# Kernel optimization log

Hardware: AMD Instinct MI355X
Metric: run time of the kernel (lower is better)

The kernel has to match this reference:

```python
import jax, jax.numpy as jnp
import numpy as np

B, L, E, H = 2, 2048, 1024, 16
HD = E // H          # head_dim = 64
G = H // 4           # heads per kernel-size group = 4


def _dwconv(x, w, b):
    """Causal depthwise conv. x: (B, G, L, D); w: (D, k); b: (D,).
    Matches PadLeft(k-1) + Conv1d(D, D, k, groups=D): y[l] = sum_j w[:, j] * x[l - (k-1) + j] + b."""
    k = w.shape[-1]
    Lx = x.shape[2]
    xp = jnp.pad(x, ((0, 0), (0, 0), (k - 1, 0), (0, 0)))
    out = b
    for j in range(k):
        out = out + xp[:, :, j:j + Lx, :] * w[:, j]
    return out


def setup_inputs() -> dict:
    key = jax.random.key(0)
    ks = jax.random.split(key, 32)
    s = 0.02
    inp = {"x": jax.random.normal(ks[0], (B, L, E), jnp.float32)}
    for i, n in enumerate(["Wq", "Wk", "Wv", "Wo"]):
        inp[n] = jax.random.normal(ks[1 + i], (E, E), jnp.float32) * s
    inp["bo"] = jax.random.normal(ks[5], (E,), jnp.float32) * s
    i = 6
    for ksz in (3, 5, 7):
        for pfx in ("q", "k", "v"):
            inp[f"{pfx}{ksz}_w"] = jax.random.normal(ks[i], (HD, ksz), jnp.float32) * (1.0 / ksz)
            inp[f"{pfx}{ksz}_b"] = jax.random.normal(ks[i + 1], (HD,), jnp.float32) * s
            i += 2
    return inp


def reference(x, Wq, Wk, Wv, Wo, bo,
              q3_w, q3_b, k3_w, k3_b, v3_w, v3_b,
              q5_w, q5_b, k5_w, k5_b, v5_w, v5_b,
              q7_w, q7_b, k7_w, k7_b, v7_w, v7_b):
    b, l, _ = x.shape

    def split(t):  # (b, l, E) -> (b, 4, G, l, HD)
        return t.reshape(b, l, 4, G, HD).transpose(0, 2, 3, 1, 4)

    q = split(x @ Wq.T)
    k = split(x @ Wk.T)
    v = split(x @ Wv.T)

    # NOTE: faithful to source quirks -- k and v convs are applied to the
    # (already convolved) q group, not to k/v.
    q0, k0, v0 = q[:, 0], k[:, 0], v[:, 0]
    q1 = _dwconv(q[:, 1], q3_w, q3_b)
    k1 = _dwconv(q1, k3_w, k3_b)
    v1 = _dwconv(q1, v3_w, v3_b)
    q2 = _dwconv(q[:, 2], q5_w, q5_b)
    k2 = _dwconv(q2, k5_w, k5_b)
    v2 = _dwconv(q2, v5_w, v5_b)
    q3 = _dwconv(q[:, 3], q7_w, q7_b)
    k3 = _dwconv(q3, k7_w, k7_b)
    v3 = _dwconv(q3, v7_w, v7_b)

    Q = jnp.concatenate([q0, q1, q2, q3], axis=1)  # (b, H, l, HD)
    K = jnp.concatenate([k0, k1, k2, k3], axis=1)
    V = jnp.concatenate([v0, v1, v2, v3], axis=1)

    logit = jnp.einsum('bnid,bnjd->bnij', Q, K) * (HD ** -0.5)
    attn = jax.nn.softmax(logit, axis=-1)
    attn_out = jnp.einsum('bnij,bnjd->bnid', attn, V)

    # Source quirk: output uses rearranged V, discarding attn_out.
    out = V.transpose(0, 2, 1, 3).reshape(b, l, E)
    # keep the attention compute alive without changing the math
    out = out + 0.0 * attn_out.transpose(0, 2, 1, 3).reshape(b, l, E)
    return out @ Wo.T + bo
```

## Files before the change

kernel.cpp:

```cpp
#include <hip/hip_runtime.h>
#include <hip/hip_bf16.h>
#include <stdint.h>

#define L_SEQ 2048
#define MTOT  4096
#define EDIM  1024

typedef __attribute__((ext_vector_type(8))) short bf16x8;
typedef __attribute__((ext_vector_type(4))) float f32x4;
typedef __attribute__((ext_vector_type(4))) float float4v;
typedef __attribute__((ext_vector_type(4))) unsigned short us4;
typedef __attribute__((ext_vector_type(2))) unsigned int u32x2;

__device__ __forceinline__ unsigned short f2b(float f) {
    union { float f; unsigned u; } v; v.f = f;
    return (unsigned short)((v.u + 0x7FFFu + ((v.u >> 16) & 1u)) >> 16);
}
__device__ __forceinline__ float b2f(unsigned short h) {
    union { unsigned u; float f; } v; v.u = ((unsigned)h) << 16;
    return v.f;
}

__device__ __forceinline__ void lds16(const void* g, void* l) {
    __builtin_amdgcn_global_load_lds((const __attribute__((address_space(1))) void*)g,
                                     (__attribute__((address_space(3))) void*)l, 16, 0, 0);
}

__global__ __launch_bounds__(256) void prep_kernel(
    const float* __restrict__ x, const float* __restrict__ Wq,
    const float* __restrict__ Wv, const float* __restrict__ Wo,
    unsigned short* __restrict__ xb, unsigned short* __restrict__ W1b,
    unsigned short* __restrict__ Wob,
    const float* __restrict__ q3w, const float* __restrict__ q3b,
    const float* __restrict__ v3w, const float* __restrict__ v3b,
    const float* __restrict__ q5w, const float* __restrict__ q5b,
    const float* __restrict__ v5w, const float* __restrict__ v5b,
    const float* __restrict__ q7w, const float* __restrict__ q7b,
    const float* __restrict__ v7w, const float* __restrict__ v7b,
    float* __restrict__ H, float* __restrict__ Beff, float* __restrict__ Corr)
{
    const int XQ = (MTOT * EDIM) / 4;
    const int WQ = (EDIM * EDIM) / 4;
    if (blockIdx.x >= 6144) {
        int ch = (blockIdx.x - 6144) * 256 + threadIdx.x;
        int g = ch >> 8;
        int d = ch & 63;
        int k = 3 + 2 * g;
        const float* qw = (g == 0) ? q3w : (g == 1) ? q5w : q7w;
        const float* qb = (g == 0) ? q3b : (g == 1) ? q5b : q7b;
        const float* vw = (g == 0) ? v3w : (g == 1) ? v5w : v7w;
        const float* vb = (g == 0) ? v3b : (g == 1) ? v5b : v7b;

        float hq[7], hv[7];
        for (int i = 0; i < 7; ++i) { hq[i] = 0.f; hv[i] = 0.f; }
        for (int i = 0; i < k; ++i) {
            hq[i] = qw[d * k + (k - 1 - i)];
            hv[i] = vw[d * k + (k - 1 - i)];
        }
        float h[13];
        for (int i = 0; i < 13; ++i) h[i] = 0.f;
        for (int a = 0; a < 7; ++a)
            for (int b = 0; b < 7; ++b)
                h[a + b] += hq[a] * hv[b];
        for (int i = 0; i < 13; ++i) H[i * 768 + ch] = h[i];

        float sv = 0.f;
        for (int j = 0; j < k; ++j) sv += vw[d * k + j];
        Beff[ch] = qb[d] * sv + vb[d];

        for (int l = 0; l < 6; ++l) {
            float s2 = 0.f;
            for (int i = l + 1; i < 7; ++i) s2 += hv[i];
            Corr[l * 768 + ch] = qb[d] * s2;
        }
        return;
    }
    int i = blockIdx.x * 256 + threadIdx.x;
    const float* src;
    unsigned short* dst;
    int j;
    if (i < XQ) {
        j = i * 4; src = x; dst = xb;
    } else if (i < XQ + WQ) {
        j = (i - XQ) * 4;
        int row = j >> 10;
        src = (row < 256) ? Wv : Wq;
        dst = W1b;
    } else {
        j = (i - XQ - WQ) * 4; src = Wo; dst = Wob;
    }
    float4v v = *(const float4v*)(src + j);
    us4 o;
    o[0] = f2b(v[0]); o[1] = f2b(v[1]); o[2] = f2b(v[2]); o[3] = f2b(v[3]);
    *(us4*)(dst + j) = o;
}

template <int OUT_MODE>
__global__ __launch_bounds__(256) void gemm_pipe(
    const unsigned short* __restrict__ A, const unsigned short* __restrict__ BT,
    unsigned short* __restrict__ Cb, float* __restrict__ Cf,
    const float* __restrict__ bias, int M, int N, int K)
{
    __shared__ unsigned short As[3][128 * 64];
    __shared__ unsigned short Bs[3][64 * 64];

    const int nbx = N >> 6;
    int orig = blockIdx.y * nbx + blockIdx.x;
    int nwg  = (M >> 7) * nbx;
    int wg   = (orig & 7) * (nwg >> 3) + (orig >> 3);
    const int m0 = (wg / nbx) * 128, n0 = (wg % nbx) * 64;

    const int tid  = threadIdx.x;
    const int wid  = tid >> 6;
    const int lane = tid & 63;
    const int wr   = wid >> 1, wc = wid & 1;
    const int fr   = lane & 15, fq = lane >> 4;
    const int swz  = fr & 7;

    f32x4 acc[4][2] = {};

    const unsigned short* Abase = A  + (size_t)m0 * K;
    const unsigned short* Bbase = BT + (size_t)n0 * K;

    auto stage = [&](int buf, int t) {
        const unsigned short* Ab = Abase + (t << 6);
        const unsigned short* Bb = Bbase + (t << 6);
#pragma unroll
        for (int i = 0; i < 4; ++i) {
            int d = wid * 256 + i * 64 + lane;
            lds16(Ab + (size_t)(d >> 3) * K + (((d & 7) ^ ((d >> 3) & 7)) * 8),
                  &As[buf][(wid * 256 + i * 64) * 8]);
        }
#pragma unroll
        for (int i = 0; i < 2; ++i) {
            int d = wid * 128 + i * 64 + lane;
            lds16(Bb + (size_t)(d >> 3) * K + (((d & 7) ^ ((d >> 3) & 7)) * 8),
                  &Bs[buf][(wid * 128 + i * 64) * 8]);
        }
    };

    auto compute = [&](int buf) {
        const unsigned short* as = As[buf];
        const unsigned short* bs = Bs[buf];
#pragma unroll
        for (int s = 0; s < 2; ++s) {
            bf16x8 a[4], b[2];
#pragma unroll
            for (int mi = 0; mi < 4; ++mi)
                a[mi] = *(const bf16x8*)(as + (wr * 64 + mi * 16 + fr) * 64
                                            + ((s * 4 + fq) ^ swz) * 8);
#pragma unroll
            for (int ni = 0; ni < 2; ++ni)
                b[ni] = *(const bf16x8*)(bs + (wc * 32 + ni * 16 + fr) * 64
                                            + ((s * 4 + fq) ^ swz) * 8);
#pragma unroll
            for (int mi = 0; mi < 4; ++mi)
#pragma unroll
                for (int ni = 0; ni < 2; ++ni)
                    acc[mi][ni] = __builtin_amdgcn_mfma_f32_16x16x32_bf16(a[mi], b[ni], acc[mi][ni], 0, 0, 0);
        }
    };

    const int NT = K >> 6;
    stage(0, 0);
    stage(1, 1);
    asm volatile("s_waitcnt vmcnt(6)" ::: "memory");
    __builtin_amdgcn_s_barrier();
    asm volatile("" ::: "memory");

    for (int t = 0; t < NT; ++t) {
        if (t + 2 < NT) stage((t + 2) % 3, t + 2);
        compute(t % 3);
        if (t + 1 < NT) {
            if (t + 2 < NT) {
                asm volatile("s_waitcnt vmcnt(6)" ::: "memory");
            } else {
                asm volatile("s_waitcnt vmcnt(0)" ::: "memory");
            }
            __builtin_amdgcn_s_barrier();
            asm volatile("" ::: "memory");
        }
    }

#pragma unroll
    for (int mi = 0; mi < 4; ++mi) {
#pragma unroll
        for (int ni = 0; ni < 2; ++ni) {
            int col  = n0 + wc * 32 + ni * 16 + fr;
            int rowb = m0 + wr * 64 + mi * 16 + fq * 4;
#pragma unroll
            for (int j = 0; j < 4; ++j) {
                float v = acc[mi][ni][j];
                if (OUT_MODE == 0) {
                    Cb[(size_t)(rowb + j) * N + col] = f2b(v);
                } else {
                    Cf[(size_t)(rowb + j) * N + col] = v + bias[col];
                }
            }
        }
    }
}

__global__ __launch_bounds__(256) void conv_kernel(
    const unsigned short* __restrict__ T, unsigned short* __restrict__ V,
    const float* __restrict__ H, const float* __restrict__ Beff,
    const float* __restrict__ Corr)
{
    int w  = blockIdx.x * 256 + threadIdx.x;
    int m  = w >> 8;
    int c4 = w & 255;
    int e0 = c4 * 4;
    const unsigned short* tp = T + (size_t)m * EDIM + e0;
    unsigned short*       vp = V + (size_t)m * EDIM + e0;
    if (e0 < 256) {
        *(u32x2*)vp = *(const u32x2*)tp;
        return;
    }
    int l  = m & (L_SEQ - 1);
    int ch = e0 - 256;
    float4v acc = *(const float4v*)(Beff + ch);
    int ni = (l < 12) ? l : 12;
    for (int i = 0; i <= ni; ++i) {
        float4v h = *(const float4v*)(H + i * 768 + ch);
        us4 t = *(const us4*)(tp - (size_t)i * EDIM);
        acc[0] += h[0] * b2f(t[0]);
        acc[1] += h[1] * b2f(t[1]);
        acc[2] += h[2] * b2f(t[2]);
        acc[3] += h[3] * b2f(t[3]);
    }
    if (l < 6) {
        float4v c = *(const float4v*)(Corr + l * 768 + ch);
        acc[0] -= c[0]; acc[1] -= c[1]; acc[2] -= c[2]; acc[3] -= c[3];
    }
    us4 o;
    o[0] = f2b(acc[0]); o[1] = f2b(acc[1]); o[2] = f2b(acc[2]); o[3] = f2b(acc[3]);
    *(us4*)vp = o;
}

extern "C" void kernel_launch(void* const* d_in, const int* in_sizes, int n_in,
                              void* d_out, int out_size, void* d_ws, size_t ws_size,
                              hipStream_t stream)
{
    const float* x  = (const float*)d_in[0];
    const float* Wq = (const float*)d_in[1];
    const float* Wv = (const float*)d_in[3];
    const float* Wo = (const float*)d_in[4];
    const float* bo = (const float*)d_in[5];

    uint8_t* ws = (uint8_t*)d_ws;
    unsigned short* xb  = (unsigned short*)(ws);
    unsigned short* W1b = (unsigned short*)(ws + (8u  << 20));
    unsigned short* Wob = (unsigned short*)(ws + (10u << 20));
    unsigned short* T   = (unsigned short*)(ws + (12u << 20));
    unsigned short* V   = (unsigned short*)(ws + (20u << 20));
    float* H    = (float*)(ws + (28u << 20));
    float* Beff = (float*)(ws + (28u << 20) + (64u << 10));
    float* Corr = (float*)(ws + (28u << 20) + (96u << 10));

    prep_kernel<<<6147, 256, 0, stream>>>(
        x, Wq, Wv, Wo, xb, W1b, Wob,
        (const float*)d_in[6],  (const float*)d_in[7],
        (const float*)d_in[10], (const float*)d_in[11],
        (const float*)d_in[12], (const float*)d_in[13],
        (const float*)d_in[16], (const float*)d_in[17],
        (const float*)d_in[18], (const float*)d_in[19],
        (const float*)d_in[22], (const float*)d_in[23],
        H, Beff, Corr);

    dim3 gg(EDIM / 64, MTOT / 128);
    gemm_pipe<0><<<gg, 256, 0, stream>>>(xb, W1b, T, nullptr, nullptr, MTOT, EDIM, EDIM);

    conv_kernel<<<4096, 256, 0, stream>>>(T, V, H, Beff, Corr);

    gemm_pipe<1><<<gg, 256, 0, stream>>>(V, Wob, nullptr, (float*)d_out, bo, MTOT, EDIM, EDIM);
}
```

Baseline: 64.26 us.

## Use 512-thread GEMM blocks and process two rows per conv thread

The GEMM keeps its 128x64 tile but moves from 4 to 8 waves per block. Each wave now owns a 32x32 sub-tile, and each thread issues three LDS async loads per stage instead of six, with the vmcnt waits adjusted to match. The conv kernel now has each thread produce two consecutive sequence rows, reusing each loaded T value for both outputs and halving the grid. The aim is more latency hiding and fewer redundant loads, at the cost of fewer MFMAs per wave and more synchronisation per unit of work.

```diff
diff --git a/kernel.cpp b/kernel.cpp
--- a/kernel.cpp
+++ b/kernel.cpp
@@ -96,7 +96,7 @@
 }
 
 template <int OUT_MODE>
-__global__ __launch_bounds__(256) void gemm_pipe(
+__global__ __launch_bounds__(512, 4) void gemm_pipe(
     const unsigned short* __restrict__ A, const unsigned short* __restrict__ BT,
     unsigned short* __restrict__ Cb, float* __restrict__ Cf,
     const float* __restrict__ bias, int M, int N, int K)
@@ -115,28 +115,23 @@
     const int lane = tid & 63;
     const int wr   = wid >> 1, wc = wid & 1;
     const int fr   = lane & 15, fq = lane >> 4;
-    const int swz  = fr & 7;
-
-    f32x4 acc[4][2] = {};
-
-    const unsigned short* Abase = A  + (size_t)m0 * K;
-    const unsigned short* Bbase = BT + (size_t)n0 * K;
+
+    f32x4 acc[2][2] = {};
+
+    const unsigned short* Aptr = A  + (size_t)m0 * K;
+    const unsigned short* Bptr = BT + (size_t)n0 * K;
+
+    const int cA1 = 512 + tid;
+    const size_t offA0 = (size_t)(tid >> 3) * K + (((tid & 7) ^ ((tid >> 3) & 7)) * 8);
+    const size_t offA1 = (size_t)(cA1 >> 3) * K + (((cA1 & 7) ^ ((cA1 >> 3) & 7)) * 8);
+    const size_t offB  = offA0;
 
     auto stage = [&](int buf, int t) {
-        const unsigned short* Ab = Abase + (t << 6);
-        const unsigned short* Bb = Bbase + (t << 6);
-#pragma unroll
-        for (int i = 0; i < 4; ++i) {
-            int d = wid * 256 + i * 64 + lane;
-            lds16(Ab + (size_t)(d >> 3) * K + (((d & 7) ^ ((d >> 3) & 7)) * 8),
-                  &As[buf][(wid * 256 + i * 64) * 8]);
-        }
-#pragma unroll
-        for (int i = 0; i < 2; ++i) {
-            int d = wid * 128 + i * 64 + lane;
-            lds16(Bb + (size_t)(d >> 3) * K + (((d & 7) ^ ((d >> 3) & 7)) * 8),
-                  &Bs[buf][(wid * 128 + i * 64) * 8]);
-        }
+        const unsigned short* Ab = Aptr + (t << 6);
+        const unsigned short* Bb = Bptr + (t << 6);
+        lds16(Ab + offA0, &As[buf][(wid * 64) * 8]);
+        lds16(Ab + offA1, &As[buf][(512 + wid * 64) * 8]);
+        lds16(Bb + offB,  &Bs[buf][(wid * 64) * 8]);
     };
 
     auto compute = [&](int buf) {
@@ -144,17 +139,19 @@
         const unsigned short* bs = Bs[buf];
 #pragma unroll
         for (int s = 0; s < 2; ++s) {
-            bf16x8 a[4], b[2];
-#pragma unroll
-            for (int mi = 0; mi < 4; ++mi)
-                a[mi] = *(const bf16x8*)(as + (wr * 64 + mi * 16 + fr) * 64
-                                            + ((s * 4 + fq) ^ swz) * 8);
-#pragma unroll
-            for (int ni = 0; ni < 2; ++ni)
-                b[ni] = *(const bf16x8*)(bs + (wc * 32 + ni * 16 + fr) * 64
-                                            + ((s * 4 + fq) ^ swz) * 8);
-#pragma unroll
-            for (int mi = 0; mi < 4; ++mi)
+            bf16x8 a[2], b[2];
+#pragma unroll
+            for (int mi = 0; mi < 2; ++mi) {
+                int row = wr * 32 + mi * 16 + fr;
+                a[mi] = *(const bf16x8*)(as + row * 64 + (((s * 4 + fq) ^ (row & 7)) * 8));
+            }
+#pragma unroll
+            for (int ni = 0; ni < 2; ++ni) {
+                int row = wc * 32 + ni * 16 + fr;
+                b[ni] = *(const bf16x8*)(bs + row * 64 + (((s * 4 + fq) ^ (row & 7)) * 8));
+            }
+#pragma unroll
+            for (int mi = 0; mi < 2; ++mi)
 #pragma unroll
                 for (int ni = 0; ni < 2; ++ni)
                     acc[mi][ni] = __builtin_amdgcn_mfma_f32_16x16x32_bf16(a[mi], b[ni], acc[mi][ni], 0, 0, 0);
@@ -164,7 +161,7 @@
     const int NT = K >> 6;
     stage(0, 0);
     stage(1, 1);
-    asm volatile("s_waitcnt vmcnt(6)" ::: "memory");
+    asm volatile("s_waitcnt vmcnt(3)" ::: "memory");
     __builtin_amdgcn_s_barrier();
     asm volatile("" ::: "memory");
 
@@ -173,7 +170,7 @@
         compute(t % 3);
         if (t + 1 < NT) {
             if (t + 2 < NT) {
-                asm volatile("s_waitcnt vmcnt(6)" ::: "memory");
+                asm volatile("s_waitcnt vmcnt(3)" ::: "memory");
             } else {
                 asm volatile("s_waitcnt vmcnt(0)" ::: "memory");
             }
@@ -183,11 +180,11 @@
     }
 
 #pragma unroll
-    for (int mi = 0; mi < 4; ++mi) {
+    for (int mi = 0; mi < 2; ++mi) {
 #pragma unroll
         for (int ni = 0; ni < 2; ++ni) {
             int col  = n0 + wc * 32 + ni * 16 + fr;
-            int rowb = m0 + wr * 64 + mi * 16 + fq * 4;
+            int rowb = m0 + wr * 32 + mi * 16 + fq * 4;
 #pragma unroll
             for (int j = 0; j < 4; ++j) {
                 float v = acc[mi][ni][j];
@@ -207,34 +204,51 @@
     const float* __restrict__ Corr)
 {
     int w  = blockIdx.x * 256 + threadIdx.x;
-    int m  = w >> 8;
-    int c4 = w & 255;
-    int e0 = c4 * 4;
+    int m  = (w >> 8) * 2;
+    int e0 = (w & 255) * 4;
     const unsigned short* tp = T + (size_t)m * EDIM + e0;
     unsigned short*       vp = V + (size_t)m * EDIM + e0;
     if (e0 < 256) {
         *(u32x2*)vp = *(const u32x2*)tp;
+        *(u32x2*)(vp + EDIM) = *(const u32x2*)(tp + EDIM);
         return;
     }
     int l  = m & (L_SEQ - 1);
     int ch = e0 - 256;
-    float4v acc = *(const float4v*)(Beff + ch);
+    float4v b4 = *(const float4v*)(Beff + ch);
+    float4v acc0 = b4, acc1 = b4;
+
+    {
+        float4v h = *(const float4v*)(H + ch);
+        us4 t = *(const us4*)(tp + EDIM);
+        acc1[0] += h[0] * b2f(t[0]); acc1[1] += h[1] * b2f(t[1]);
+        acc1[2] += h[2] * b2f(t[2]); acc1[3] += h[3] * b2f(t[3]);
+    }
     int ni = (l < 12) ? l : 12;
     for (int i = 0; i <= ni; ++i) {
-        float4v h = *(const float4v*)(H + i * 768 + ch);
         us4 t = *(const us4*)(tp - (size_t)i * EDIM);
-        acc[0] += h[0] * b2f(t[0]);
-        acc[1] += h[1] * b2f(t[1]);
-        acc[2] += h[2] * b2f(t[2]);
-        acc[3] += h[3] * b2f(t[3]);
+        float4v h0 = *(const float4v*)(H + i * 768 + ch);
+        acc0[0] += h0[0] * b2f(t[0]); acc0[1] += h0[1] * b2f(t[1]);
+        acc0[2] += h0[2] * b2f(t[2]); acc0[3] += h0[3] * b2f(t[3]);
+        if (i < 12) {
+            float4v h1 = *(const float4v*)(H + (i + 1) * 768 + ch);
+            acc1[0] += h1[0] * b2f(t[0]); acc1[1] += h1[1] * b2f(t[1]);
+            acc1[2] += h1[2] * b2f(t[2]); acc1[3] += h1[3] * b2f(t[3]);
+        }
     }
     if (l < 6) {
         float4v c = *(const float4v*)(Corr + l * 768 + ch);
-        acc[0] -= c[0]; acc[1] -= c[1]; acc[2] -= c[2]; acc[3] -= c[3];
-    }
-    us4 o;
-    o[0] = f2b(acc[0]); o[1] = f2b(acc[1]); o[2] = f2b(acc[2]); o[3] = f2b(acc[3]);
-    *(us4*)vp = o;
+        acc0[0] -= c[0]; acc0[1] -= c[1]; acc0[2] -= c[2]; acc0[3] -= c[3];
+    }
+    if (l + 1 < 6) {
+        float4v c = *(const float4v*)(Corr + (l + 1) * 768 + ch);
+        acc1[0] -= c[0]; acc1[1] -= c[1]; acc1[2] -= c[2]; acc1[3] -= c[3];
+    }
+    us4 o0, o1;
+    o0[0] = f2b(acc0[0]); o0[1] = f2b(acc0[1]); o0[2] = f2b(acc0[2]); o0[3] = f2b(acc0[3]);
+    o1[0] = f2b(acc1[0]); o1[1] = f2b(acc1[1]); o1[2] = f2b(acc1[2]); o1[3] = f2b(acc1[3]);
+    *(us4*)vp = o0;
+    *(us4*)(vp + EDIM) = o1;
 }
 
 extern "C" void kernel_launch(void* const* d_in, const int* in_sizes, int n_in,
@@ -268,9 +282,9 @@
         H, Beff, Corr);
 
     dim3 gg(EDIM / 64, MTOT / 128);
-    gemm_pipe<0><<<gg, 256, 0, stream>>>(xb, W1b, T, nullptr, nullptr, MTOT, EDIM, EDIM);
-
-    conv_kernel<<<4096, 256, 0, stream>>>(T, V, H, Beff, Corr);
-
-    gemm_pipe<1><<<gg, 256, 0, stream>>>(V, Wob, nullptr, (float*)d_out, bo, MTOT, EDIM, EDIM);
-}
+    gemm_pipe<0><<<gg, 512, 0, stream>>>(xb, W1b, T, nullptr, nullptr, MTOT, EDIM, EDIM);
+
+    conv_kernel<<<2048, 256, 0, stream>>>(T, V, H, Beff, Corr);
+
+    gemm_pipe<1><<<gg, 512, 0, stream>>>(V, Wob, nullptr, (float*)d_out, bo, MTOT, EDIM, EDIM);
+}
```

New measurement: 57.72 us. 1.11x faster.
